# Optimization experiments

Measured on AMD Instinct MI355X. Metric: run time of the kernel, lower is better.

The kernel has to match this reference:

```python
import jax, jax.numpy as jnp
import numpy as np

DIM = 1024
HEADS = 16
HEAD_DIM = DIM // HEADS
SEQ_TGT = 2048  # query length
SEQ_SRC = 1024  # key/value length
BATCH = 4
LN_EPS = 1e-5


def setup_inputs() -> dict:
    key = jax.random.key(0)
    ks = jax.random.split(key, 8)
    s = 1.0 / np.sqrt(DIM)
    return {
        "q": jax.random.normal(ks[0], (BATCH, SEQ_TGT, DIM), dtype=jnp.float32),
        "kv": jax.random.normal(ks[1], (BATCH, SEQ_SRC, DIM), dtype=jnp.float32),
        "Wq": jax.random.normal(ks[2], (DIM, DIM), dtype=jnp.float32) * s,
        "Wk": jax.random.normal(ks[3], (DIM, DIM), dtype=jnp.float32) * s,
        "Wv": jax.random.normal(ks[4], (DIM, DIM), dtype=jnp.float32) * s,
        "Wo": jax.random.normal(ks[5], (DIM, DIM), dtype=jnp.float32) * s,
        "bo": jnp.zeros((DIM,), dtype=jnp.float32),
        "ln_g": jnp.ones((DIM,), dtype=jnp.float32),
        "ln_b": jnp.zeros((DIM,), dtype=jnp.float32),
    }


def _split_heads(x):
    b, n, _ = x.shape
    return x.reshape(b, n, HEADS, HEAD_DIM).transpose(0, 2, 1, 3)  # b h n d


def reference(q, kv, Wq, Wk, Wv, Wo, bo, ln_g, ln_b):
    # QKV projections (torch Linear: x @ W.T, no bias)
    qh = _split_heads(q @ Wq.T)    # [b,h,Nq,d]
    kh = _split_heads(kv @ Wk.T)   # [b,h,Nk,d]
    vh = _split_heads(kv @ Wv.T)   # [b,h,Nk,d]

    scale = HEAD_DIM ** -0.5
    qk = jnp.einsum('bhid,bhjd->bhij', qh, kh) * scale  # [b,h,Nq,Nk]

    # Block-causal mask: base [Nk,Nk] causal mask repeat_interleaved along query
    # axis by downscaling = Nq // Nk. Equivalent to allow iff (i // downscaling) >= j.
    downscaling = SEQ_TGT // SEQ_SRC  # = 2, upscaled_dim = 0
    i = jnp.arange(SEQ_TGT)[:, None]
    j = jnp.arange(SEQ_SRC)[None, :]
    neg_inf = jnp.asarray(-jnp.inf, dtype=qk.dtype)
    mask = jnp.where((i // downscaling) >= j, jnp.asarray(0.0, qk.dtype), neg_inf)

    attn = jax.nn.softmax(qk + mask[None, None, :, :], axis=-1)
    out = jnp.einsum('bhij,bhjd->bhid', attn, vh)           # [b,h,Nq,d]
    out = out.transpose(0, 2, 1, 3).reshape(BATCH, SEQ_TGT, DIM)

    # LayerNorm (norm_out=True)
    mu = jnp.mean(out, axis=-1, keepdims=True)
    var = jnp.mean(jnp.square(out - mu), axis=-1, keepdims=True)
    out = (out - mu) * jax.lax.rsqrt(var + LN_EPS) * ln_g + ln_b

    # Output projection (dropout is identity in eval mode)
    return out @ Wo.T + bo
```

## Files before the change

kernel.cpp:

```cpp
#include <hip/hip_runtime.h>

typedef unsigned short u16;
typedef unsigned int   u32;

typedef __bf16 bf16x8 __attribute__((ext_vector_type(8)));
typedef __bf16 bf16x4 __attribute__((ext_vector_type(4)));
typedef float  f32x4  __attribute__((ext_vector_type(4)));

__device__ __forceinline__ float bf2f(u16 v) {
    u32 u = ((u32)v) << 16; float f; __builtin_memcpy(&f, &u, 4); return f;
}
__device__ __forceinline__ u16 f2bf(float f) {
    __bf16 h = (__bf16)f; u16 r; __builtin_memcpy(&r, &h, 2); return r;
}

__device__ __forceinline__ void gload_lds16(const void* g, void* l) {
    __builtin_amdgcn_global_load_lds(
        (const __attribute__((address_space(1))) u32*)g,
        (__attribute__((address_space(3))) u32*)l, 16, 0, 0);
}

__device__ __forceinline__ void barrier_raw() {
    __builtin_amdgcn_s_barrier();
    asm volatile("" ::: "memory");
}

#define QSCALE 0.1803368801111204f

__global__ __launch_bounds__(256) void cvt_all(
    const float* __restrict__ q, const float* __restrict__ kv,
    const float* __restrict__ Wq, const float* __restrict__ Wk,
    const float* __restrict__ Wv, const float* __restrict__ Wo,
    u16* __restrict__ dst)
{
    const int total = 16 << 18;
    int i = blockIdx.x * 256 + threadIdx.x;
    const int stride = gridDim.x * 256;
    for (; i < total; i += stride) {
        int seg = i >> 18;
        const float* s; int off;
        if (seg < 8)        { s = q;  off = i; }
        else if (seg < 12)  { s = kv; off = i - (8 << 18); }
        else if (seg == 12) { s = Wq; off = i & 262143; }
        else if (seg == 13) { s = Wk; off = i & 262143; }
        else if (seg == 14) { s = Wv; off = i & 262143; }
        else                { s = Wo; off = i & 262143; }
        float4 v = reinterpret_cast<const float4*>(s)[off];
        ushort4 o;
        o.x = f2bf(v.x); o.y = f2bf(v.y); o.z = f2bf(v.z); o.w = f2bf(v.w);
        reinterpret_cast<ushort4*>(dst)[i] = o;
    }
}

template<int KK, int MH, bool RB>
__device__ __forceinline__ void qkv_phase(
    const char* ldsb, int d, int ha, int hb, int rbB, int fr, int fq,
    bf16x8 (&bF)[4], f32x4 (&acc)[8][4])
{
    const int sw = ((KK * 4 + fq) ^ (fr & 7)) * 16;
    if (RB) {
        #pragma unroll
        for (int ni = 0; ni < 4; ni++)
            bF[ni] = *reinterpret_cast<const bf16x8*>(
                ldsb + 65536 + d * 32768 + hb * 16384 + (rbB + ni * 16 + fr) * 128 + sw);
    }
    bf16x8 aF[4];
    #pragma unroll
    for (int j = 0; j < 4; j++)
        aF[j] = *reinterpret_cast<const bf16x8*>(
            ldsb + d * 32768 + ha * 16384 + ((MH * 4 + j) * 16 + fr) * 128 + sw);
    __builtin_amdgcn_s_setprio(1);
    #pragma unroll
    for (int j = 0; j < 4; j++)
        #pragma unroll
        for (int ni = 0; ni < 4; ni++)
            acc[MH * 4 + j][ni] = __builtin_amdgcn_mfma_f32_16x16x32_bf16(
                aF[j], bF[ni], acc[MH * 4 + j][ni], 0, 0, 0);
    __builtin_amdgcn_s_setprio(0);
}

__global__ __launch_bounds__(512, 2) void gemm_qkv8(
    const u16* __restrict__ q8, const u16* __restrict__ kv8,
    const u16* __restrict__ Wq8, const u16* __restrict__ Wk8,
    const u16* __restrict__ Wv8,
    u16* __restrict__ Qb, u16* __restrict__ Kb, u16* __restrict__ Vb)
{
    __shared__ __align__(16) u16 lds[65536];
    char* ldsb = (char*)lds;

    const int tid = threadIdx.x;
    const int l = tid & 63, w = tid >> 6;
    const int fr = l & 15, fq = l >> 4;

    const int bid = (int)blockIdx.x;
    const int lbid = (bid & 7) * 32 + (bid >> 3);
    const u16 *A, *W; u16* C; float scale = 1.0f; int rt, ct;
    if (lbid < 128)      { A = q8;  W = Wq8; C = Qb; scale = QSCALE; rt = lbid >> 2; ct = lbid & 3; }
    else if (lbid < 192) { int t = lbid - 128; A = kv8; W = Wk8; C = Kb; rt = t >> 2; ct = t & 3; }
    else                 { int t = lbid - 192; A = kv8; W = Wv8; C = Vb; rt = t >> 2; ct = t & 3; }
    const int brow = rt * 256, bcol = ct * 256;

    const int wr = (w >> 2) * 128, wc = (w & 3) * 64;
    const int ha = w >> 2;
    const int hb = (w & 3) >> 1;
    const int rbB = wc & 64;

    const int srow = l >> 3;
    const int sslot = (l & 7) ^ srow;

    const u16* srcA[2][2];
    const u16* srcB[2][2];
    #pragma unroll
    for (int h = 0; h < 2; h++)
        #pragma unroll
        for (int i = 0; i < 2; i++) {
            int grow = h * 128 + (2 * w + i) * 8 + srow;
            srcA[h][i] = A + (size_t)(brow + grow) * 1024 + sslot * 8;
            srcB[h][i] = W + (size_t)(bcol + grow) * 1024 + sslot * 8;
        }

    auto stageA = [&](int kt, int d) {
        #pragma unroll
        for (int h = 0; h < 2; h++)
            #pragma unroll
            for (int i = 0; i < 2; i++)
                gload_lds16(srcA[h][i] + kt * 64,
                            ldsb + d * 32768 + h * 16384 + (2 * w + i) * 1024);
    };
    auto stageBh = [&](int kt, int d, int h) {
        #pragma unroll
        for (int i = 0; i < 2; i++)
            gload_lds16(srcB[h][i] + kt * 64,
                        ldsb + 65536 + d * 32768 + h * 16384 + (2 * w + i) * 1024);
    };

    f32x4 acc[8][4] = {};

    stageA(0, 0); stageBh(0, 0, 0); stageBh(0, 0, 1);
    asm volatile("s_waitcnt vmcnt(0)" ::: "memory");
    barrier_raw();

    for (int kt = 0; kt < 16; ++kt) {
        const int d = kt & 1, nd = d ^ 1;
        const bool pre = (kt < 15);
        bf16x8 bF[4];

        if (pre) stageA(kt + 1, nd);
        qkv_phase<0, 0, true >(ldsb, d, ha, hb, rbB, fr, fq, bF, acc);
        barrier_raw();
        if (pre) stageBh(kt + 1, nd, 0);
        qkv_phase<0, 1, false>(ldsb, d, ha, hb, rbB, fr, fq, bF, acc);
        barrier_raw();
        if (pre) stageBh(kt + 1, nd, 1);
        qkv_phase<1, 0, true >(ldsb, d, ha, hb, rbB, fr, fq, bF, acc);
        barrier_raw();
        qkv_phase<1, 1, false>(ldsb, d, ha, hb, rbB, fr, fq, bF, acc);
        asm volatile("s_waitcnt vmcnt(0)" ::: "memory");
        barrier_raw();
    }

    #pragma unroll
    for (int mi = 0; mi < 8; mi++) {
        int row = brow + wr + mi * 16 + fq * 4;
        #pragma unroll
        for (int ni = 0; ni < 4; ni++) {
            int col = bcol + wc + ni * 16 + fr;
            #pragma unroll
            for (int r = 0; r < 4; r++)
                C[(size_t)(row + r) * 1024 + col] = f2bf(acc[mi][ni][r] * scale);
        }
    }
}

__global__ __launch_bounds__(512, 1) void gemm_out8(
    const u16* __restrict__ A, const u16* __restrict__ W,
    const float* __restrict__ bias, float* __restrict__ C)
{
    __shared__ __align__(16) u16 lds[49152];
    char* ldsb = (char*)lds;

    const int tid = threadIdx.x;
    const int l = tid & 63, w = tid >> 6;
    const int fr = l & 15, fq = l >> 4;

    const int bid = (int)blockIdx.x;
    const int lbid = (bid & 7) * 32 + (bid >> 3);
    const int rt = lbid >> 2, ct = lbid & 3;
    const int brow = rt * 128, bcol = ct * 256;

    const int wr = (w >> 2) * 64, wc = (w & 3) * 64;
    const int hb = (w & 3) >> 1;
    const int rbB = wc & 64;

    const int srow = l >> 3;
    const int sslot = (l & 7) ^ srow;

    const u16* srcA[2];
    const u16* srcB[2][2];
    #pragma unroll
    for (int i = 0; i < 2; i++) {
        int grow = (2 * w + i) * 8 + srow;
        srcA[i] = A + (size_t)(brow + grow) * 1024 + sslot * 8;
    }
    #pragma unroll
    for (int h = 0; h < 2; h++)
        #pragma unroll
        for (int i = 0; i < 2; i++) {
            int grow = h * 128 + (2 * w + i) * 8 + srow;
            srcB[h][i] = W + (size_t)(bcol + grow) * 1024 + sslot * 8;
        }

    auto stageA = [&](int kt, int d) {
        #pragma unroll
        for (int i = 0; i < 2; i++)
            gload_lds16(srcA[i] + kt * 64, ldsb + d * 16384 + (2 * w + i) * 1024);
    };
    auto stageB = [&](int kt, int d) {
        #pragma unroll
        for (int h = 0; h < 2; h++)
            #pragma unroll
            for (int i = 0; i < 2; i++)
                gload_lds16(srcB[h][i] + kt * 64,
                            ldsb + 32768 + d * 32768 + h * 16384 + (2 * w + i) * 1024);
    };

    f32x4 acc[4][4] = {};

    stageA(0, 0); stageB(0, 0);
    asm volatile("s_waitcnt vmcnt(0)" ::: "memory");
    barrier_raw();

    for (int kt = 0; kt < 16; ++kt) {
        const int d = kt & 1, nd = d ^ 1;
        const bool pre = (kt < 15);

        if (pre) stageA(kt + 1, nd);
        #pragma unroll
        for (int kk = 0; kk < 2; kk++) {
            const int sw = ((kk * 4 + fq) ^ (fr & 7)) * 16;
            bf16x8 aF[4], bF[4];
            #pragma unroll
            for (int j = 0; j < 4; j++)
                aF[j] = *reinterpret_cast<const bf16x8*>(
                    ldsb + d * 16384 + ((wr + j * 16 + fr) & 127) * 128 + sw);
            #pragma unroll
            for (int ni = 0; ni < 4; ni++)
                bF[ni] = *reinterpret_cast<const bf16x8*>(
                    ldsb + 32768 + d * 32768 + hb * 16384
                    + (rbB + ni * 16 + fr) * 128 + sw);
            __builtin_amdgcn_s_setprio(1);
            #pragma unroll
            for (int j = 0; j < 4; j++)
                #pragma unroll
                for (int ni = 0; ni < 4; ni++)
                    acc[j][ni] = __builtin_amdgcn_mfma_f32_16x16x32_bf16(
                        aF[j], bF[ni], acc[j][ni], 0, 0, 0);
            __builtin_amdgcn_s_setprio(0);
            if (kk == 0) {
                barrier_raw();
                if (pre) stageB(kt + 1, nd);
            }
        }
        asm volatile("s_waitcnt vmcnt(0)" ::: "memory");
        barrier_raw();
    }

    #pragma unroll
    for (int mi = 0; mi < 4; mi++) {
        int row = brow + wr + mi * 16 + fq * 4;
        #pragma unroll
        for (int ni = 0; ni < 4; ni++) {
            int col = bcol + wc + ni * 16 + fr;
            float bv = bias[col];
            #pragma unroll
            for (int r = 0; r < 4; r++)
                C[(size_t)(row + r) * 1024 + col] = acc[mi][ni][r] + bv;
        }
    }
}

__global__ __launch_bounds__(256) void attn_kernel(
    const u16* __restrict__ Q, const u16* __restrict__ K,
    const u16* __restrict__ V, u16* __restrict__ O)
{
    __shared__ __align__(16) u16 smem[25600];
    u16* Ks = smem;
    u16* Vt = smem + 8192;
    u16* Ps = smem + 16384;
    float* Ow = (float*)smem;

    const int tid = threadIdx.x;
    const int l = tid & 63, w = tid >> 6;
    const int fr = l & 15, fq = l >> 4;

    const int id = (int)blockIdx.x;
    const int bh = (id & 7) | ((id >> 6) << 3);
    const int px = (id >> 3) & 7;
    const int b = bh >> 4, h = bh & 15;

    const int kp = tid & 31, d0 = (tid >> 5) * 8;
    const int kr = l >> 3, ksw = l & 7;
    u16* Pw = Ps + w * (32 * 72);

    const u16* Kbh = K + (size_t)b * 1024 * 1024 + h * 64;
    const u16* Vbh = V + (size_t)b * 1024 * 1024 + h * 64;

    bf16x8 ones;
    #pragma unroll
    for (int i = 0; i < 8; i++) ones[i] = (__bf16)1.0f;

    for (int half = 0; half < 2; ++half) {
        const int bq = half ? px : 15 - px;
        const int q0 = bq * 128;

        if (half) __syncthreads();

        bf16x8 qf[2][2];
        #pragma unroll
        for (int n = 0; n < 2; n++) {
            size_t qoff = (size_t)(b * 2048 + q0 + w * 32 + n * 16 + fr) * 1024 + h * 64;
            qf[n][0] = *reinterpret_cast<const bf16x8*>(Q + qoff + fq * 8);
            qf[n][1] = *reinterpret_cast<const bf16x8*>(Q + qoff + 32 + fq * 8);
        }

        f32x4 sumac[2] = {};
        f32x4 of[4][2] = {};

        {
            #pragma unroll
            for (int i = 0; i < 2; i++) {
                int cI = w * 2 + i;
                int r = cI * 8 + kr;
                gload_lds16(Kbh + (size_t)r * 1024 + ((ksw ^ (r & 7)) * 8), &Ks[cI * 512]);
            }
            const u16* vp = Vbh + (size_t)(2 * kp) * 1024 + d0;
            uint4 ra = *reinterpret_cast<const uint4*>(vp);
            uint4 rb = *reinterpret_cast<const uint4*>(vp + 1024);
            u16 ea[8], eb[8];
            __builtin_memcpy(ea, &ra, 16);
            __builtin_memcpy(eb, &rb, 16);
            #pragma unroll
            for (int jd = 0; jd < 8; jd++) {
                int d = d0 + jd;
                u32 pk = (u32)ea[jd] | ((u32)eb[jd] << 16);
                *(u32*)((char*)Vt + d * 128 + (((kp >> 2) ^ (d & 7)) * 16) + (kp & 3) * 4) = pk;
            }
        }
        __syncthreads();

        int cur = 0;
        for (int t = 0; t <= bq; ++t) {
            const bool pre = (t < bq);
            uint4 ra, rb;
            if (pre) {
                const int j0n = (t + 1) * 64;
                #pragma unroll
                for (int i = 0; i < 2; i++) {
                    int cI = w * 2 + i;
                    int r = cI * 8 + kr;
                    gload_lds16(Kbh + (size_t)(j0n + r) * 1024 + ((ksw ^ (r & 7)) * 8),
                                &Ks[(cur ^ 1) * 4096 + cI * 512]);
                }
                const u16* vp = Vbh + (size_t)(j0n + 2 * kp) * 1024 + d0;
                ra = *reinterpret_cast<const uint4*>(vp);
                rb = *reinterpret_cast<const uint4*>(vp + 1024);
            }

            f32x4 sf[4][2] = {};
            #pragma unroll
            for (int kk = 0; kk < 2; kk++) {
                bf16x8 kf[4];
                #pragma unroll
                for (int m = 0; m < 4; m++) {
                    int key = m * 16 + fr;
                    kf[m] = *reinterpret_cast<const bf16x8*>(
                        (char*)Ks + cur * 8192 + key * 128 + (((kk * 4 + fq) ^ (key & 7)) * 16));
                }
                #pragma unroll
                for (int m = 0; m < 4; m++)
                    #pragma unroll
                    for (int n = 0; n < 2; n++)
                        sf[m][n] = __builtin_amdgcn_mfma_f32_16x16x32_bf16(
                            kf[m], qf[n][kk], sf[m][n], 0, 0, 0);
            }

            const bool diag = (t == bq);
            #pragma unroll
            for (int m = 0; m < 4; m++)
                #pragma unroll
                for (int n = 0; n < 2; n++)
                    #pragma unroll
                    for (int r = 0; r < 4; r++) {
                        float s = sf[m][n][r];
                        if (diag) {
                            int kl = m * 16 + fq * 4 + r;
                            int ql = w * 32 + n * 16 + fr;
                            if (kl > (ql >> 1)) s = -1e30f;
                        }
                        sf[m][n][r] = __builtin_amdgcn_exp2f(s);
                    }

            #pragma unroll
            for (int m = 0; m < 4; m++)
                #pragma unroll
                for (int n = 0; n < 2; n++) {
                    bf16x4 pk;
                    pk[0] = (__bf16)sf[m][n][0]; pk[1] = (__bf16)sf[m][n][1];
                    pk[2] = (__bf16)sf[m][n][2]; pk[3] = (__bf16)sf[m][n][3];
                    int q = n * 16 + fr;
                    *(bf16x4*)((char*)Pw + q * 144 + m * 32 + fq * 8) = pk;
                }

            #pragma unroll
            for (int kk = 0; kk < 2; kk++) {
                bf16x8 pf[2], vf[4];
                #pragma unroll
                for (int n = 0; n < 2; n++) {
                    int q = n * 16 + fr;
                    pf[n] = *reinterpret_cast<const bf16x8*>(
                        (char*)Pw + q * 144 + kk * 64 + fq * 16);
                }
                #pragma unroll
                for (int m = 0; m < 4; m++) {
                    int d = m * 16 + fr;
                    vf[m] = *reinterpret_cast<const bf16x8*>(
                        (char*)Vt + cur * 8192 + d * 128 + (((kk * 4 + fq) ^ (d & 7)) * 16));
                }
                #pragma unroll
                for (int m = 0; m < 4; m++)
                    #pragma unroll
                    for (int n = 0; n < 2; n++)
                        of[m][n] = __builtin_amdgcn_mfma_f32_16x16x32_bf16(
                            vf[m], pf[n], of[m][n], 0, 0, 0);
                #pragma unroll
                for (int n = 0; n < 2; n++)
                    sumac[n] = __builtin_amdgcn_mfma_f32_16x16x32_bf16(
                        ones, pf[n], sumac[n], 0, 0, 0);
            }

            if (pre) {
                u16 ea[8], eb[8];
                __builtin_memcpy(ea, &ra, 16);
                __builtin_memcpy(eb, &rb, 16);
                #pragma unroll
                for (int jd = 0; jd < 8; jd++) {
                    int d = d0 + jd;
                    u32 pk = (u32)ea[jd] | ((u32)eb[jd] << 16);
                    *(u32*)((char*)Vt + (cur ^ 1) * 8192 + d * 128
                            + (((kp >> 2) ^ (d & 7)) * 16) + (kp & 3) * 4) = pk;
                }
            }
            __syncthreads();
            cur ^= 1;
        }

        float* OwW = Ow + w * (32 * 68);
        #pragma unroll
        for (int m = 0; m < 4; m++)
            #pragma unroll
            for (int n = 0; n < 2; n++) {
                f32x4 v = of[m][n] * (1.0f / sumac[n][0]);
                int q = n * 16 + fr;
                *reinterpret_cast<f32x4*>(&OwW[q * 68 + m * 16 + fq * 4]) = v;
            }
        {
            int ql = l >> 1, dh = l & 1;
            size_t grow = (size_t)(b * 2048 + q0 + w * 32 + ql) * 1024 + h * 64 + dh * 32;
            #pragma unroll
            for (int p = 0; p < 4; p++) {
                f32x4 a = *reinterpret_cast<const f32x4*>(&OwW[ql * 68 + dh * 32 + p * 8]);
                f32x4 c = *reinterpret_cast<const f32x4*>(&OwW[ql * 68 + dh * 32 + p * 8 + 4]);
                bf16x8 pk;
                pk[0]=(__bf16)a[0]; pk[1]=(__bf16)a[1]; pk[2]=(__bf16)a[2]; pk[3]=(__bf16)a[3];
                pk[4]=(__bf16)c[0]; pk[5]=(__bf16)c[1]; pk[6]=(__bf16)c[2]; pk[7]=(__bf16)c[3];
                *reinterpret_cast<bf16x8*>(O + grow + p * 8) = pk;
            }
        }
    }
}

__global__ __launch_bounds__(256) void ln_kernel(
    u16* __restrict__ buf, const float* __restrict__ g, const float* __restrict__ beta)
{
    const int row = blockIdx.x, tid = threadIdx.x;
    const size_t base = (size_t)row * 1024;
    ushort4 v = *reinterpret_cast<const ushort4*>(&buf[base + tid * 4]);
    float x0 = bf2f(v.x), x1 = bf2f(v.y), x2 = bf2f(v.z), x3 = bf2f(v.w);
    float s = x0 + x1 + x2 + x3;
    float q = x0 * x0 + x1 * x1 + x2 * x2 + x3 * x3;
    #pragma unroll
    for (int d = 32; d; d >>= 1) { s += __shfl_xor(s, d); q += __shfl_xor(q, d); }
    __shared__ float sm[8];
    int w = tid >> 6, l = tid & 63;
    if (l == 0) { sm[w] = s; sm[4 + w] = q; }
    __syncthreads();
    s = sm[0] + sm[1] + sm[2] + sm[3];
    q = sm[4] + sm[5] + sm[6] + sm[7];
    float mean = s * (1.0f / 1024.0f);
    float var = q * (1.0f / 1024.0f) - mean * mean;
    float rstd = rsqrtf(var + 1e-5f);
    float4 gv = *reinterpret_cast<const float4*>(&g[tid * 4]);
    float4 bv = *reinterpret_cast<const float4*>(&beta[tid * 4]);
    ushort4 o;
    o.x = f2bf((x0 - mean) * rstd * gv.x + bv.x);
    o.y = f2bf((x1 - mean) * rstd * gv.y + bv.y);
    o.z = f2bf((x2 - mean) * rstd * gv.z + bv.z);
    o.w = f2bf((x3 - mean) * rstd * gv.w + bv.w);
    *reinterpret_cast<ushort4*>(&buf[base + tid * 4]) = o;
}

extern "C" void kernel_launch(void* const* d_in, const int* in_sizes, int n_in,
                              void* d_out, int out_size, void* d_ws, size_t ws_size,
                              hipStream_t stream)
{
    const float* q    = (const float*)d_in[0];
    const float* kv   = (const float*)d_in[1];
    const float* Wq   = (const float*)d_in[2];
    const float* Wk   = (const float*)d_in[3];
    const float* Wv   = (const float*)d_in[4];
    const float* Wo   = (const float*)d_in[5];
    const float* bo   = (const float*)d_in[6];
    const float* ln_g = (const float*)d_in[7];
    const float* ln_b = (const float*)d_in[8];

    const size_t MQ = (size_t)8192 * 1024;
    const size_t MK = (size_t)4096 * 1024;
    const size_t MW = (size_t)1024 * 1024;

    u16* q8  = (u16*)d_ws;
    u16* kv8 = q8 + MQ;
    u16* Wq8 = kv8 + MK;
    u16* Wk8 = Wq8 + MW;
    u16* Wv8 = Wk8 + MW;
    u16* Wo8 = Wv8 + MW;
    u16* Qb  = Wo8 + MW;
    u16* Kb  = Qb + MQ;
    u16* Vb  = Kb + MK;
    u16* Ab  = Vb + MK;

    cvt_all<<<2048, 256, 0, stream>>>(q, kv, Wq, Wk, Wv, Wo, q8);
    gemm_qkv8<<<256, 512, 0, stream>>>(q8, kv8, Wq8, Wk8, Wv8, Qb, Kb, Vb);
    attn_kernel<<<512, 256, 0, stream>>>(Qb, Kb, Vb, Ab);
    ln_kernel<<<8192, 256, 0, stream>>>(Ab, ln_g, ln_b);
    gemm_out8<<<256, 512, 0, stream>>>(Ab, Wo8, bo, (float*)d_out);
}
```

Measured before the change: 121.1 us.

## Fold LayerNorm into output GEMM epilogue via row stats and folded weights

Removes the separate LayerNorm kernel. The attention kernel now writes per-row, per-head partial sums and sums of squares. gamma is folded into Wo during conversion, and per-column sums S1 = Wo·g and SB = Wo·beta + bo are precomputed. The output GEMM reduces the row statistics and applies mean and rstd in its epilogue. This saves a full read-modify-write pass over the attention output and one launch, but the statistics come from fp32 values while the GEMM consumes bf16-rounded unnormalized activations, which shifts numerics slightly.

After: 122.9 us. Within noise of the previous version (+1.5%).

```diff
diff --git a/kernel.cpp b/kernel.cpp
--- a/kernel.cpp
+++ b/kernel.cpp
@@ -31,24 +31,54 @@
     const float* __restrict__ q, const float* __restrict__ kv,
     const float* __restrict__ Wq, const float* __restrict__ Wk,
     const float* __restrict__ Wv, const float* __restrict__ Wo,
-    u16* __restrict__ dst)
+    const float* __restrict__ g, const float* __restrict__ be,
+    const float* __restrict__ bo,
+    u16* __restrict__ dst, float* __restrict__ S1, float* __restrict__ SB)
 {
-    const int total = 16 << 18;
-    int i = blockIdx.x * 256 + threadIdx.x;
-    const int stride = gridDim.x * 256;
-    for (; i < total; i += stride) {
-        int seg = i >> 18;
-        const float* s; int off;
-        if (seg < 8)        { s = q;  off = i; }
-        else if (seg < 12)  { s = kv; off = i - (8 << 18); }
-        else if (seg == 12) { s = Wq; off = i & 262143; }
-        else if (seg == 13) { s = Wk; off = i & 262143; }
-        else if (seg == 14) { s = Wv; off = i & 262143; }
-        else                { s = Wo; off = i & 262143; }
-        float4 v = reinterpret_cast<const float4*>(s)[off];
-        ushort4 o;
-        o.x = f2bf(v.x); o.y = f2bf(v.y); o.z = f2bf(v.z); o.w = f2bf(v.w);
-        reinterpret_cast<ushort4*>(dst)[i] = o;
+    const int bid = (int)blockIdx.x;
+    if (bid < 2048) {
+        const int total = 16 << 18;
+        int i = bid * 256 + threadIdx.x;
+        const int stride = 2048 * 256;
+        for (; i < total; i += stride) {
+            int seg = i >> 18;
+            const float* s; int off = i & 262143;
+            bool isWo = false;
+            if (seg < 8)        { s = q;  off = i; }
+            else if (seg < 12)  { s = kv; off = i - (8 << 18); }
+            else if (seg == 12) { s = Wq; }
+            else if (seg == 13) { s = Wk; }
+            else if (seg == 14) { s = Wv; }
+            else                { s = Wo; isWo = true; }
+            float4 v = reinterpret_cast<const float4*>(s)[off];
+            if (isWo) {
+                float4 g4 = reinterpret_cast<const float4*>(g)[off & 255];
+                v.x *= g4.x; v.y *= g4.y; v.z *= g4.z; v.w *= g4.w;
+            }
+            ushort4 o;
+            o.x = f2bf(v.x); o.y = f2bf(v.y); o.z = f2bf(v.z); o.w = f2bf(v.w);
+            reinterpret_cast<ushort4*>(dst)[i] = o;
+        }
+    } else {
+        const int n = (bid - 2048) * 4 + (threadIdx.x >> 6);
+        const int l = threadIdx.x & 63;
+        const float4* wrow = reinterpret_cast<const float4*>(Wo + (size_t)n * 1024);
+        float s1 = 0.f, sb = 0.f;
+        #pragma unroll
+        for (int j = 0; j < 4; j++) {
+            int c4 = j * 64 + l;
+            float4 wv = wrow[c4];
+            float4 g4 = reinterpret_cast<const float4*>(g)[c4];
+            float4 b4 = reinterpret_cast<const float4*>(be)[c4];
+            s1 += wv.x * g4.x + wv.y * g4.y + wv.z * g4.z + wv.w * g4.w;
+            sb += wv.x * b4.x + wv.y * b4.y + wv.z * b4.z + wv.w * b4.w;
+        }
+        #pragma unroll
+        for (int d = 1; d < 64; d <<= 1) {
+            s1 += __shfl_xor(s1, d);
+            sb += __shfl_xor(sb, d);
+        }
+        if (l == 0) { S1[n] = s1; SB[n] = sb + bo[n]; }
     }
 }
 
@@ -174,9 +204,12 @@
 
 __global__ __launch_bounds__(512, 1) void gemm_out8(
     const u16* __restrict__ A, const u16* __restrict__ W,
-    const float* __restrict__ bias, float* __restrict__ C)
+    const float2* __restrict__ rowpart, const float* __restrict__ S1,
+    const float* __restrict__ SB, float* __restrict__ C)
 {
     __shared__ __align__(16) u16 lds[49152];
+    __shared__ float2 rtmp[512];
+    __shared__ float2 rowst[128];
     char* ldsb = (char*)lds;
 
     const int tid = threadIdx.x;
@@ -187,6 +220,25 @@
     const int lbid = (bid & 7) * 32 + (bid >> 3);
     const int rt = lbid >> 2, ct = lbid & 3;
     const int brow = rt * 128, bcol = ct * 256;
+
+    {
+        int lrow = tid >> 2, grp = tid & 3;
+        const float2* rp = rowpart + (size_t)(brow + lrow) * 16 + grp * 4;
+        float sx = 0.f, sq = 0.f;
+        #pragma unroll
+        for (int j = 0; j < 4; j++) { float2 p = rp[j]; sx += p.x; sq += p.y; }
+        rtmp[tid] = make_float2(sx, sq);
+    }
+    __syncthreads();
+    if (tid < 128) {
+        float sx = 0.f, sq = 0.f;
+        #pragma unroll
+        for (int j = 0; j < 4; j++) { float2 p = rtmp[tid * 4 + j]; sx += p.x; sq += p.y; }
+        float mu = sx * (1.0f / 1024.0f);
+        float var = sq * (1.0f / 1024.0f) - mu * mu;
+        rowst[tid] = make_float2(mu, rsqrtf(var + 1e-5f));
+    }
+    __syncthreads();
 
     const int wr = (w >> 2) * 64, wc = (w & 3) * 64;
     const int hb = (w & 3) >> 1;
@@ -267,21 +319,26 @@
 
     #pragma unroll
     for (int mi = 0; mi < 4; mi++) {
-        int row = brow + wr + mi * 16 + fq * 4;
+        int lr0 = wr + mi * 16 + fq * 4;
+        int row = brow + lr0;
         #pragma unroll
         for (int ni = 0; ni < 4; ni++) {
             int col = bcol + wc + ni * 16 + fr;
-            float bv = bias[col];
-            #pragma unroll
-            for (int r = 0; r < 4; r++)
-                C[(size_t)(row + r) * 1024 + col] = acc[mi][ni][r] + bv;
+            float s1c = S1[col];
+            float sbc = SB[col];
+            #pragma unroll
+            for (int r = 0; r < 4; r++) {
+                float2 st = rowst[lr0 + r];
+                C[(size_t)(row + r) * 1024 + col] =
+                    st.y * (acc[mi][ni][r] - st.x * s1c) + sbc;
+            }
         }
     }
 }
 
 __global__ __launch_bounds__(256) void attn_kernel(
     const u16* __restrict__ Q, const u16* __restrict__ K,
-    const u16* __restrict__ V, u16* __restrict__ O)
+    const u16* __restrict__ V, u16* __restrict__ O, float2* __restrict__ rowpart)
 {
     __shared__ __align__(16) u16 smem[25600];
     u16* Ks = smem;
@@ -455,14 +512,33 @@
         }
 
         float* OwW = Ow + w * (32 * 68);
-        #pragma unroll
-        for (int m = 0; m < 4; m++)
-            #pragma unroll
-            for (int n = 0; n < 2; n++) {
-                f32x4 v = of[m][n] * (1.0f / sumac[n][0]);
+        float psum[2] = {0.f, 0.f}, psq[2] = {0.f, 0.f};
+        #pragma unroll
+        for (int n = 0; n < 2; n++) {
+            float inv = 1.0f / sumac[n][0];
+            #pragma unroll
+            for (int m = 0; m < 4; m++) {
+                f32x4 v = of[m][n] * inv;
                 int q = n * 16 + fr;
                 *reinterpret_cast<f32x4*>(&OwW[q * 68 + m * 16 + fq * 4]) = v;
-            }
+                psum[n] += v[0] + v[1] + v[2] + v[3];
+                psq[n]  += v[0]*v[0] + v[1]*v[1] + v[2]*v[2] + v[3]*v[3];
+            }
+        }
+        #pragma unroll
+        for (int n = 0; n < 2; n++) {
+            psum[n] += __shfl_xor(psum[n], 16);
+            psum[n] += __shfl_xor(psum[n], 32);
+            psq[n]  += __shfl_xor(psq[n], 16);
+            psq[n]  += __shfl_xor(psq[n], 32);
+        }
+        if (fq == 0) {
+            #pragma unroll
+            for (int n = 0; n < 2; n++) {
+                size_t grow = (size_t)(b * 2048 + q0 + w * 32 + n * 16 + fr);
+                rowpart[grow * 16 + h] = make_float2(psum[n], psq[n]);
+            }
+        }
         {
             int ql = l >> 1, dh = l & 1;
             size_t grow = (size_t)(b * 2048 + q0 + w * 32 + ql) * 1024 + h * 64 + dh * 32;
@@ -477,36 +553,6 @@
             }
         }
     }
-}
-
-__global__ __launch_bounds__(256) void ln_kernel(
-    u16* __restrict__ buf, const float* __restrict__ g, const float* __restrict__ beta)
-{
-    const int row = blockIdx.x, tid = threadIdx.x;
-    const size_t base = (size_t)row * 1024;
-    ushort4 v = *reinterpret_cast<const ushort4*>(&buf[base + tid * 4]);
-    float x0 = bf2f(v.x), x1 = bf2f(v.y), x2 = bf2f(v.z), x3 = bf2f(v.w);
-    float s = x0 + x1 + x2 + x3;
-    float q = x0 * x0 + x1 * x1 + x2 * x2 + x3 * x3;
-    #pragma unroll
-    for (int d = 32; d; d >>= 1) { s += __shfl_xor(s, d); q += __shfl_xor(q, d); }
-    __shared__ float sm[8];
-    int w = tid >> 6, l = tid & 63;
-    if (l == 0) { sm[w] = s; sm[4 + w] = q; }
-    __syncthreads();
-    s = sm[0] + sm[1] + sm[2] + sm[3];
-    q = sm[4] + sm[5] + sm[6] + sm[7];
-    float mean = s * (1.0f / 1024.0f);
-    float var = q * (1.0f / 1024.0f) - mean * mean;
-    float rstd = rsqrtf(var + 1e-5f);
-    float4 gv = *reinterpret_cast<const float4*>(&g[tid * 4]);
-    float4 bv = *reinterpret_cast<const float4*>(&beta[tid * 4]);
-    ushort4 o;
-    o.x = f2bf((x0 - mean) * rstd * gv.x + bv.x);
-    o.y = f2bf((x1 - mean) * rstd * gv.y + bv.y);
-    o.z = f2bf((x2 - mean) * rstd * gv.z + bv.z);
-    o.w = f2bf((x3 - mean) * rstd * gv.w + bv.w);
-    *reinterpret_cast<ushort4*>(&buf[base + tid * 4]) = o;
 }
 
 extern "C" void kernel_launch(void* const* d_in, const int* in_sizes, int n_in,
@@ -537,10 +583,13 @@
     u16* Kb  = Qb + MQ;
     u16* Vb  = Kb + MK;
     u16* Ab  = Vb + MK;
-
-    cvt_all<<<2048, 256, 0, stream>>>(q, kv, Wq, Wk, Wv, Wo, q8);
+    float* S1 = (float*)(Ab + MQ);
+    float* SB = S1 + 1024;
+    float2* rowpart = (float2*)q8;
+
+    cvt_all<<<2304, 256, 0, stream>>>(q, kv, Wq, Wk, Wv, Wo, ln_g, ln_b, bo,
+                                      q8, S1, SB);
     gemm_qkv8<<<256, 512, 0, stream>>>(q8, kv8, Wq8, Wk8, Wv8, Qb, Kb, Vb);
-    attn_kernel<<<512, 256, 0, stream>>>(Qb, Kb, Vb, Ab);
-    ln_kernel<<<8192, 256, 0, stream>>>(Ab, ln_g, ln_b);
-    gemm_out8<<<256, 512, 0, stream>>>(Ab, Wo8, bo, (float*)d_out);
-}
+    attn_kernel<<<512, 256, 0, stream>>>(Qb, Kb, Vb, Ab, rowpart);
+    gemm_out8<<<256, 512, 0, stream>>>(Ab, Wo8, rowpart, S1, SB, (float*)d_out);
+}
```
